# Optimization experiments

Measured on AMD Instinct MI355X. Metric: run time of the kernel, lower is better.

## Reference

```python
import jax, jax.numpy as jnp
import numpy as np

N_REGION = 36
N_PARTIAL = 5
SMOOTH = 9.0
EPS = 1e-8
BN_EPS = 1e-5
LN_EPS = 1e-5


def l2norm(x, axis=-1):
    return x / (jnp.sqrt(jnp.sum(x * x, axis=axis, keepdims=True)) + EPS)


def _uniform_linear(key, fan_in, fan_out):
    r = float(np.sqrt(6.0) / np.sqrt(fan_in + fan_out))
    return jax.random.uniform(key, (fan_in, fan_out), minval=-r, maxval=r, dtype=jnp.float32)


def setup_inputs() -> dict:
    key = jax.random.key(0)
    D, S = 1024, 256
    NI, NC, NW = 64, 32, 40
    ks = jax.random.split(key, 16)
    return {
        "img_emb": jax.random.normal(ks[0], (NI, N_REGION, D), jnp.float32),
        "cap_emb": jax.random.normal(ks[1], (NC, NW, D), jnp.float32),
        "cap_lens": jnp.full((NC,), NW, dtype=jnp.int32),
        "adjs": jax.random.randint(ks[2], (NI, N_REGION, N_REGION), 0, 2).astype(jnp.int32),
        "depends": jnp.zeros((NC, 2), jnp.int32),
        # TextSA (t_global_w)
        "tsa_lw": _uniform_linear(ks[3], D, D), "tsa_lb": jnp.zeros((D,), jnp.float32),
        "tsa_gw": _uniform_linear(ks[4], D, D), "tsa_gb": jnp.zeros((D,), jnp.float32),
        "tsa_cw": _uniform_linear(ks[5], D, 1), "tsa_cb": jnp.zeros((1,), jnp.float32),
        # VisualSA block
        "vl_w": _uniform_linear(ks[6], D, D), "vl_b": jnp.zeros((D,), jnp.float32),
        "vbn_lg": jnp.ones((N_REGION,), jnp.float32), "vbn_lb": jnp.zeros((N_REGION,), jnp.float32),
        "vg_w": _uniform_linear(ks[7], D, D), "vg_b": jnp.zeros((D,), jnp.float32),
        "vbn_gg": jnp.ones((D,), jnp.float32), "vbn_gb": jnp.zeros((D,), jnp.float32),
        "vc_w": _uniform_linear(ks[8], D, 1), "vc_b": jnp.zeros((1,), jnp.float32),
        # similarity heads
        "loc_w": _uniform_linear(ks[9], D, S), "loc_b": jnp.zeros((S,), jnp.float32),
        "par_w": _uniform_linear(ks[10], D, S), "par_b": jnp.zeros((S,), jnp.float32),
        "glo_w": _uniform_linear(ks[11], D, S), "glo_b": jnp.zeros((S,), jnp.float32),
        "sim_w": _uniform_linear(ks[12], S, 1), "sim_b": jnp.zeros((1,), jnp.float32),
        "ln_g": jnp.ones((N_REGION,), jnp.float32), "ln_b": jnp.zeros((N_REGION,), jnp.float32),
    }


def reference(img_emb, cap_emb, cap_lens, adjs, depends,
              tsa_lw, tsa_lb, tsa_gw, tsa_gb, tsa_cw, tsa_cb,
              vl_w, vl_b, vbn_lg, vbn_lb, vg_w, vg_b, vbn_gg, vbn_gb, vc_w, vc_b,
              loc_w, loc_b, par_w, par_b, glo_w, glo_b, sim_w, sim_b, ln_g, ln_b):
    # cap_lens: all captions use the full (uniform) length; depends unused (as in original forward).
    B, R, D = img_emb.shape
    # ---- global image embedding (VisualSA; dropout=identity, BN uses batch stats) ----
    img_ave = img_emb.mean(axis=1)                                    # (B,D)
    h = img_emb @ vl_w + vl_b                                         # (B,R,D)
    mu = h.mean(axis=(0, 2), keepdims=True)
    var = h.var(axis=(0, 2), keepdims=True)
    l_emb = jnp.tanh((h - mu) / jnp.sqrt(var + BN_EPS) * vbn_lg[None, :, None] + vbn_lb[None, :, None])
    g = img_ave @ vg_w + vg_b                                         # (B,D)
    g_emb = jnp.tanh((g - g.mean(0)) / jnp.sqrt(g.var(0) + BN_EPS) * vbn_gg + vbn_gb)
    common = l_emb * g_emb[:, None, :]
    weights_raw = common @ vc_w + vc_b                                # (B,R,1)
    w = jax.nn.softmax(weights_raw[..., 0], axis=-1)[..., None]
    new_global = (w * img_emb).sum(axis=1)                            # (B,D)
    norm_glo = jnp.sqrt(jnp.sum(new_global ** 2, axis=-1, keepdims=True)) + EPS  # (B,1)
    img_glo = new_global / norm_glo                                   # (B,D)
    # ---- partial image embeddings (collect_emb, expressed as direct gather) ----
    vals, idx = jax.lax.top_k(adjs, N_PARTIAL)                        # (B,R,K)
    self_idx = jnp.broadcast_to(jnp.arange(R)[None, :, None], idx.shape)
    eff = jnp.where(vals == 1, idx, self_idx)                         # (B,R,K)
    bidx = jnp.arange(B)[:, None, None]
    feat_g = img_emb[bidx, eff]                                       # (B,R,K,D)
    wg = jax.nn.softmax(weights_raw[bidx, eff][..., 0], axis=-1)[..., None]  # (B,R,K,1)
    img_par = (wg * feat_g).sum(axis=2) / norm_glo[:, None, :]        # (B,R,D)

    def per_cap(cap_i):                                               # cap_i: (NW,D)
        # TextSA global caption embedding (dropout=identity)
        cap_ave = cap_i.mean(axis=0)
        le = jnp.tanh(cap_i @ tsa_lw + tsa_lb)                        # (NW,D)
        ge = jnp.tanh(cap_ave @ tsa_gw + tsa_gb)                      # (D,)
        cw = jax.nn.softmax((le * ge) @ tsa_cw[:, 0] + tsa_cb[0], axis=0)
        cap_glo = l2norm((cw[:, None] * cap_i).sum(axis=0))           # (D,)
        # SCAN attention: query=img_emb, context=caption words (shared across images)
        attn = jnp.einsum('nd,brd->bnr', cap_i, img_emb)              # (B,NW,R)
        attn = jax.nn.leaky_relu(attn, 0.1)
        attn = l2norm(attn, axis=2)
        attn = jax.nn.softmax(attn.transpose(0, 2, 1) * SMOOTH, axis=2)  # (B,R,NW)
        ctx = l2norm(jnp.einsum('brn,nd->brd', attn, cap_i))          # (B,R,D)
        sim_loc = l2norm(jax.nn.relu((ctx - img_emb) ** 2 @ loc_w + loc_b))        # (B,R,S)
        sim_par = l2norm(jax.nn.relu((img_par - cap_glo) ** 2 @ par_w + par_b))    # (B,R,S)
        sim_glo = l2norm(jax.nn.relu((img_glo - cap_glo) ** 2 @ glo_w + glo_b))    # (B,S)
        similarity = sim_par * sim_glo[:, None, :]
        wts = (similarity @ sim_w)[..., 0] + sim_b[0]                 # (B,R)
        m = wts.mean(axis=-1, keepdims=True)
        v = wts.var(axis=-1, keepdims=True)
        wts = jax.nn.sigmoid((wts - m) / jnp.sqrt(v + LN_EPS) * ln_g + ln_b)
        sim_loc = wts[..., None] * sim_loc
        sim_emb = jnp.concatenate([sim_glo[:, None, :], sim_loc], axis=1)  # (B,R+1,S)
        return sim_emb, sim_glo

    sim_emb_v, sim_glo_v = jax.vmap(per_cap)(cap_emb)                 # (NC,B,R+1,S), (NC,B,S)
    return sim_emb_v, sim_glo_v
```

## Files before the change

kernel.cpp:

```cpp
#include <hip/hip_runtime.h>

typedef unsigned short u16;
typedef __attribute__((ext_vector_type(8))) short short8;
typedef __attribute__((ext_vector_type(4))) float f32x4;

#define BN_ 64
#define CN_ 32
#define WN_ 40
#define RN_ 36
#define DN_ 1024
#define SN_ 256
#define KN_ 5
#define EPS_ 1e-8f
#define BNE_ 1e-5f
#define LNE_ 1e-5f
#define SMOOTH_ 9.0f

__device__ __forceinline__ float bf2f(u16 u){ return __uint_as_float(((unsigned)u)<<16); }
__device__ __forceinline__ u16 f2bf(float f){
  unsigned u = __float_as_uint(f);
  u += 0x7fffu + ((u>>16)&1u);
  return (u16)(u>>16);
}
__device__ __forceinline__ float ldf(const void* p, size_t i, int mode){
  return mode ? ((const float*)p)[i] : bf2f(((const u16*)p)[i]);
}
__device__ __forceinline__ void stf(void* p, size_t i, float v, int mode){
  if (mode) ((float*)p)[i] = v; else ((u16*)p)[i] = f2bf(v);
}
__device__ __forceinline__ int get_mode(const unsigned* oneflag){
  return (oneflag[0] == 0x3F800000u) ? 1 : 0;
}
__device__ __forceinline__ short8 ld_frag8(const void* p, size_t elem, int mode){
  if (mode == 0){
    union { uint4 u; short8 s; } cv;
    cv.u = *(const uint4*)((const u16*)p + elem);
    return cv.s;
  } else {
    const float* f = (const float*)p;
    short8 r;
#pragma unroll
    for (int j=0;j<8;j++) r[j] = (short)f2bf(f[elem+j]);
    return r;
  }
}

__device__ __forceinline__ float wave_sum(float v){
#pragma unroll
  for (int off=32; off>0; off>>=1) v += __shfl_down(v, off, 64);
  return v;
}
__device__ float block_sum(float v, float* sc4){
  v = wave_sum(v);
  if ((threadIdx.x & 63)==0) sc4[threadIdx.x>>6] = v;
  __syncthreads();
  float r = sc4[0]+sc4[1]+sc4[2]+sc4[3];
  __syncthreads();
  return r;
}

__global__ void mean_k(const void* X, float* out, int G, int L, float inv, const unsigned* oneflag){
  int mode = get_mode(oneflag);
  int idx = blockIdx.x*256 + threadIdx.x;
  if (idx >= G*DN_) return;
  int g = idx >> 10, d = idx & 1023;
  size_t base = (size_t)g*L*DN_ + d;
  float s = 0.f;
  for (int l=0; l<L; l++) s += ldf(X, base + (size_t)l*DN_, mode);
  out[idx] = s*inv;
}

__global__ void prep_w_k(const void* W, u16* WT, int nlog2, const unsigned* oneflag){
  int mode = get_mode(oneflag);
  int N = 1 << nlog2;
  int idx = blockIdx.x*256 + threadIdx.x;
  if (idx >= (DN_<<nlog2)) return;
  int k = idx >> nlog2, n = idx & (N-1);
  float v = ldf(W, idx, mode);
  WT[(((size_t)(k>>6))*N + n)*64 + (k&63)] = f2bf(v);
}

__global__ __launch_bounds__(256) void gemm_nt_mfma_k(
    const void* A, const void* B, int bt, const u16* WT,
    const void* bias, int has_bias, int act, const unsigned* oneflag,
    float* C, int M, int N, int K){
  int mode = get_mode(oneflag);
  int t = threadIdx.x;
  int w = t>>6, lane = t&63, q = lane>>4, cm = lane&15;
  int m0 = blockIdx.y*64, n0 = blockIdx.x*64 + w*16;
  f32x4 acc[4];
#pragma unroll
  for (int mt=0;mt<4;mt++) acc[mt] = (f32x4){0.f,0.f,0.f,0.f};
  int nkt = K>>6;
  for (int kt=0; kt<nkt; kt++){
#pragma unroll
    for (int ks=0; ks<2; ks++){
      int kb = kt*64 + ks*32 + q*8;
      short8 b;
      if (bt) b = ld_frag8(B, (size_t)(n0+cm)*K + kb, mode);
      else {
        union { uint4 u; short8 s; } cv;
        cv.u = *(const uint4*)(WT + (((size_t)kt*N + n0+cm)*64 + ks*32 + q*8));
        b = cv.s;
      }
#pragma unroll
      for (int mt=0; mt<4; mt++){
        short8 a = ld_frag8(A, (size_t)(m0+mt*16+cm)*K + kb, mode);
        acc[mt] = __builtin_amdgcn_mfma_f32_16x16x32_bf16(a, b, acc[mt], 0,0,0);
      }
    }
  }
  float bv = has_bias ? ldf(bias, n0+cm, mode) : 0.f;
#pragma unroll
  for (int mt=0; mt<4; mt++){
#pragma unroll
    for (int r=0; r<4; r++){
      int m = m0 + mt*16 + q*4 + r;
      float v = acc[mt][r] + bv;
      if (act==1) v = tanhf(v);
      C[(size_t)m*N + n0+cm] = v;
    }
  }
}

__global__ void bnl_sum_k(const float* h, float* bnp){
  __shared__ float sc[4];
  int r = blockIdx.x>>3, bg = blockIdx.x&7;
  float s=0.f, s2=0.f;
  for (int bb=0; bb<8; bb++){
    int b = bg*8+bb;
    const float* p = h + ((size_t)b*RN_ + r)*DN_;
    for (int d=threadIdx.x; d<DN_; d+=256){ float x=p[d]; s+=x; s2+=x*x; }
  }
  s  = block_sum(s,  sc);
  s2 = block_sum(s2, sc);
  if (threadIdx.x==0){ bnp[blockIdx.x*2]=s; bnp[blockIdx.x*2+1]=s2; }
}
__global__ void bnl_apply_k(float* h, const void* gg_, const void* bb_,
                            const float* bnp, const unsigned* oneflag){
  int mode = get_mode(oneflag);
  int row = blockIdx.x; int r = row % RN_;
  float s=0.f, s2=0.f;
  for (int j=0;j<8;j++){ s += bnp[(r*8+j)*2]; s2 += bnp[(r*8+j)*2+1]; }
  float inv = 1.f/(float)(BN_*DN_);
  float mu = s*inv;
  float var = s2*inv - mu*mu;
  float rstd = rsqrtf(var + BNE_);
  float gg = ldf(gg_, r, mode), bb = ldf(bb_, r, mode);
  float* p = h + (size_t)row*DN_;
  for (int d=threadIdx.x; d<DN_; d+=256) p[d] = tanhf((p[d]-mu)*rstd*gg + bb);
}

__global__ void bn_global_k(float* g, const void* gg_, const void* bb_, const unsigned* oneflag){
  int mode = get_mode(oneflag);
  int d = blockIdx.x*256 + threadIdx.x;
  if (d >= DN_) return;
  float s=0.f, s2=0.f;
  for (int b=0;b<BN_;b++){ float x=g[(size_t)b*DN_+d]; s+=x; s2+=x*x; }
  float m = s/(float)BN_;
  float var = s2/(float)BN_ - m*m;
  float rstd = rsqrtf(var + BNE_);
  float ga=ldf(gg_,d,mode), be=ldf(bb_,d,mode);
  for (int b=0;b<BN_;b++){
    size_t i=(size_t)b*DN_+d;
    g[i] = tanhf((g[i]-m)*rstd*ga + be);
  }
}

__global__ void gemm_k(const void* A, int a_ws, const void* B, int transb,
                       const void* bias, int has_bias, int act,
                       const unsigned* oneflag, float* C, int M, int N, int K){
  __shared__ float As[32][33];
  __shared__ float Bs[32][33];
  int mode = get_mode(oneflag);
  int n0 = blockIdx.x*32, m0 = blockIdx.y*32;
  int tid = threadIdx.x;
  int tx = tid & 15, ty = tid >> 4;
  float a00=0,a01=0,a10=0,a11=0;
  for (int kt=0; kt<K; kt+=32){
    for (int l=0; l<4; l++){
      int idx = tid + l*256;
      {
        int i = idx >> 5, k = idx & 31;
        int m = m0 + i;
        float v = 0.f;
        if (m < M){
          size_t off = (size_t)m*K + kt + k;
          v = a_ws ? ((const float*)A)[off] : ldf(A, off, mode);
        }
        As[i][k] = v;
      }
      if (!transb){
        int k = idx >> 5, j = idx & 31;
        int n = n0 + j;
        Bs[k][j] = (n<N) ? ldf(B, (size_t)(kt+k)*N + n, mode) : 0.f;
      } else {
        int j = idx >> 5, k = idx & 31;
        int n = n0 + j;
        Bs[k][j] = (n<N) ? ldf(B, (size_t)n*K + kt + k, mode) : 0.f;
      }
    }
    __syncthreads();
#pragma unroll
    for (int kk=0; kk<32; kk++){
      float x0 = As[ty][kk], x1 = As[ty+16][kk];
      float y0 = Bs[kk][tx], y1 = Bs[kk][tx+16];
      a00 += x0*y0; a01 += x0*y1; a10 += x1*y0; a11 += x1*y1;
    }
    __syncthreads();
  }
  float acc[2][2] = {{a00,a01},{a10,a11}};
  for (int i=0;i<2;i++){
    for (int j=0;j<2;j++){
      int m = m0 + ty + i*16, n = n0 + tx + j*16;
      if (m<M && n<N){
        float v = acc[i][j];
        if (has_bias) v += ldf(bias, n, mode);
        if (act==1) v = tanhf(v);
        C[(size_t)m*N + n] = v;
      }
    }
  }
}

__global__ void wraw_k(const float* lemb, const float* gemb, const void* vc_w, const void* vc_b,
                       float* wraw, const unsigned* oneflag){
  __shared__ float sc[4];
  int mode = get_mode(oneflag);
  int br = blockIdx.x; int b = br / RN_;
  const float* lp = lemb + (size_t)br*DN_;
  const float* gp = gemb + (size_t)b*DN_;
  float s=0.f;
  for (int d=threadIdx.x; d<DN_; d+=256) s += lp[d]*gp[d]*ldf(vc_w,d,mode);
  s = block_sum(s, sc);
  if (threadIdx.x==0) wraw[br] = s + ldf(vc_b,0,mode);
}

__global__ void glo_k(const float* wraw, const void* img, float* img_glo, float* rnorm,
                      const unsigned* oneflag){
  __shared__ float sc[4];
  __shared__ float wsm[RN_];
  __shared__ float srn;
  int mode = get_mode(oneflag);
  int b = blockIdx.x;
  if (threadIdx.x==0){
    float mx=-1e30f;
    for (int r=0;r<RN_;r++) mx = fmaxf(mx, wraw[b*RN_+r]);
    float sum=0.f;
    for (int r=0;r<RN_;r++){ float e=expf(wraw[b*RN_+r]-mx); wsm[r]=e; sum+=e; }
    float inv=1.f/sum;
    for (int r=0;r<RN_;r++) wsm[r]*=inv;
  }
  __syncthreads();
  float ng[4]; float s2=0.f;
#pragma unroll
  for (int j=0;j<4;j++){
    int d = threadIdx.x + j*256;
    float s=0.f;
    for (int r=0;r<RN_;r++) s += wsm[r]*ldf(img, ((size_t)b*RN_+r)*DN_ + d, mode);
    ng[j]=s; s2 += s*s;
  }
  s2 = block_sum(s2, sc);
  if (threadIdx.x==0) srn = 1.f/(sqrtf(s2)+EPS_);
  __syncthreads();
  float rn = srn;
#pragma unroll
  for (int j=0;j<4;j++) img_glo[(size_t)b*DN_ + threadIdx.x + j*256] = ng[j]*rn;
  if (threadIdx.x==0) rnorm[b]=rn;
}

__global__ void partial_k(const float* wraw, const int* adjs, const void* img,
                          const float* rnorm, u16* img_parh, const unsigned* oneflag){
  __shared__ float wg[KN_];
  __shared__ int eff[KN_];
  int mode = get_mode(oneflag);
  int br = blockIdx.x; int b = br / RN_; int r = br % RN_;
  if (threadIdx.x==0){
    int cnt=0;
    const int* ap = adjs + (size_t)br*RN_;
    for (int j=0;j<RN_ && cnt<KN_;j++) if (ap[j]==1) eff[cnt++]=j;
    for (int k=cnt;k<KN_;k++) eff[k]=r;
    float v[KN_]; float mx=-1e30f;
    for (int k=0;k<KN_;k++){ v[k]=wraw[b*RN_+eff[k]]; mx=fmaxf(mx,v[k]); }
    float sum=0.f;
    for (int k=0;k<KN_;k++){ v[k]=expf(v[k]-mx); sum+=v[k]; }
    float inv=1.f/sum;
    for (int k=0;k<KN_;k++) wg[k]=v[k]*inv;
  }
  __syncthreads();
  float rn = rnorm[b];
  for (int d=threadIdx.x; d<DN_; d+=256){
    float s=0.f;
#pragma unroll
    for (int k=0;k<KN_;k++) s += wg[k]*ldf(img, ((size_t)b*RN_+eff[k])*DN_ + d, mode);
    img_parh[(size_t)br*DN_ + d] = f2bf(s*rn);
  }
}

__global__ void capglo_k(const float* le, const float* ge, const void* tsa_cw, const void* tsa_cb,
                         const void* cap, float* cap_glo, const unsigned* oneflag){
  __shared__ float sc[4];
  __shared__ float score[WN_];
  __shared__ float srn;
  int mode = get_mode(oneflag);
  int c = blockIdx.x;
  int t = threadIdx.x;
  float gw[4];
#pragma unroll
  for (int j=0;j<4;j++){ int d=t+j*256; gw[j] = ge[(size_t)c*DN_+d]*ldf(tsa_cw,d,mode); }
  float cb0 = ldf(tsa_cb,0,mode);
  for (int n=0;n<WN_;n++){
    const float* lp = le + ((size_t)c*WN_+n)*DN_;
    float s=0.f;
#pragma unroll
    for (int j=0;j<4;j++) s += lp[t+j*256]*gw[j];
    s = block_sum(s, sc);
    if (t==0) score[n] = s + cb0;
  }
  __syncthreads();
  if (t==0){
    float mx=-1e30f;
    for (int n=0;n<WN_;n++) mx=fmaxf(mx,score[n]);
    float sum=0.f;
    for (int n=0;n<WN_;n++){ float e=expf(score[n]-mx); score[n]=e; sum+=e; }
    float inv=1.f/sum;
    for (int n=0;n<WN_;n++) score[n]*=inv;
  }
  __syncthreads();
  float v[4]; float s2=0.f;
#pragma unroll
  for (int j=0;j<4;j++){
    int d=t+j*256;
    float s=0.f;
    for (int n=0;n<WN_;n++) s += score[n]*ldf(cap, ((size_t)c*WN_+n)*DN_ + d, mode);
    v[j]=s; s2+=s*s;
  }
  s2 = block_sum(s2, sc);
  if (t==0) srn = 1.f/(sqrtf(s2)+EPS_);
  __syncthreads();
#pragma unroll
  for (int j=0;j<4;j++) cap_glo[(size_t)c*DN_ + t + j*256] = v[j]*srn;
}

__global__ void attn_norm_k(float* attn){
  __shared__ float buf[BN_*RN_];
  int row = blockIdx.x;
  int t = threadIdx.x;
  float* p = attn + (size_t)row*(BN_*RN_);
  for (int i=t; i<BN_*RN_; i+=256){
    float x = p[i];
    buf[i] = (x>=0.f)? x : 0.1f*x;
  }
  __syncthreads();
  if (t < BN_){
    float s2=0.f;
#pragma unroll
    for (int r=0;r<RN_;r++){ float x=buf[t*RN_+r]; s2+=x*x; }
    float rn = 1.f/(sqrtf(s2)+EPS_);
#pragma unroll
    for (int r=0;r<RN_;r++) buf[t*RN_+r] *= rn;
  }
  __syncthreads();
  for (int i=t; i<BN_*RN_; i+=256) p[i] = buf[i];
}

__global__ void gram_k(const void* cap, float* gram, const unsigned* oneflag){
  __shared__ float capS[WN_][128];
  int mode = get_mode(oneflag);
  int c = blockIdx.x, t = threadIdx.x;
  float acc[7];
  int pi[7], pj[7];
#pragma unroll
  for (int u=0; u<7; u++){
    acc[u]=0.f;
    int p = t + u*256;
    pi[u] = p/40; pj[u] = p%40;
    if (pi[u] >= WN_) pi[u] = 0;
  }
  for (int k0=0; k0<DN_; k0+=128){
    for (int i=t; i<WN_*128; i+=256){
      int n = i>>7, kk = i&127;
      capS[n][kk] = ldf(cap, ((size_t)c*WN_+n)*DN_ + k0+kk, mode);
    }
    __syncthreads();
#pragma unroll
    for (int u=0; u<7; u++){
      if (t + u*256 < 1600){
        float s=0.f;
        for (int kk=0; kk<128; kk++) s += capS[pi[u]][kk]*capS[pj[u]][kk];
        acc[u] += s;
      }
    }
    __syncthreads();
  }
#pragma unroll
  for (int u=0; u<7; u++)
    if (t + u*256 < 1600) gram[(size_t)c*1600 + t + u*256] = acc[u];
}

__global__ void simglo_k(const float* img_glo, const float* cap_glo, const void* glo_w,
                         const void* glo_b, float* simglo_ws, void* out, const unsigned* oneflag){
  __shared__ float X[DN_];
  __shared__ float sc[4];
  __shared__ float srn;
  int mode = get_mode(oneflag);
  int cb = blockIdx.x; int c = cb >> 6; int b = cb & 63;
  int t = threadIdx.x;
#pragma unroll
  for (int j=0;j<4;j++){
    int d=t+j*256;
    float dif = img_glo[(size_t)b*DN_+d] - cap_glo[(size_t)c*DN_+d];
    X[d] = dif*dif;
  }
  __syncthreads();
  float acc=0.f;
  for (int k=0;k<DN_;k++) acc += X[k]*ldf(glo_w, (size_t)k*SN_ + t, mode);
  acc += ldf(glo_b, t, mode);
  acc = fmaxf(acc, 0.f);
  float s2 = block_sum(acc*acc, sc);
  if (t==0) srn = 1.f/(sqrtf(s2)+EPS_);
  __syncthreads();
  float o = acc*srn;
  simglo_ws[(size_t)cb*SN_ + t] = o;
  stf(out, (size_t)cb*37*SN_ + t, o, mode);
  stf(out, (size_t)CN_*BN_*37*SN_ + (size_t)cb*SN_ + t, o, mode);
}

__global__ __launch_bounds__(256) void wts_mfma_k(const u16* img_parh, const float* cap_glo,
    const u16* WT, const void* par_b, const float* simglo, const void* sim_w,
    const void* sim_b, float* wts_raw, const unsigned* oneflag){
  __shared__ uint4 AsV[2][512];
  __shared__ float red[4][64];
  __shared__ float rns[64];
  int mode = get_mode(oneflag);
  int t = threadIdx.x;
  int rows0 = blockIdx.x*64;
  int c = rows0 / (BN_*RN_);
  int br0 = rows0 % (BN_*RN_);
  int w = t>>6, lane = t&63, q = lane>>4, cm = lane&15;
  f32x4 acc[4][4];
#pragma unroll
  for (int mt=0;mt<4;mt++)
#pragma unroll
    for (int nt=0;nt<4;nt++) acc[mt][nt] = (f32x4){0.f,0.f,0.f,0.f};

  for (int kt=0; kt<16; kt++){
    int p = kt&1;
#pragma unroll
    for (int h=0; h<2; h++){
      int fi = t + h*256;
      int mt = fi>>7, ks=(fi>>6)&1, ln=fi&63;
      int fq = ln>>4, fcm = ln&15;
      int row = mt*16+fcm;
      int kb = kt*64 + ks*32 + fq*8;
      union { uint4 u; u16 s[8]; } pv;
      pv.u = *(const uint4*)(img_parh + (size_t)(br0+row)*DN_ + kb);
      const float* cg = cap_glo + (size_t)c*DN_ + kb;
      union { uint4 u; u16 s[8]; } xs;
#pragma unroll
      for (int j=0;j<8;j++){ float d = bf2f(pv.s[j]) - cg[j]; xs.s[j] = f2bf(d*d); }
      AsV[p][fi & 511] = xs.u;
    }
    __syncthreads();
#pragma unroll
    for (int ks=0; ks<2; ks++){
      short8 a[4];
#pragma unroll
      for (int mt=0; mt<4; mt++){
        union { uint4 u; short8 s; } cv;
        cv.u = AsV[p][(mt*2+ks)*64 + lane];
        a[mt] = cv.s;
      }
#pragma unroll
      for (int nt=0; nt<4; nt++){
        int n = w*64 + nt*16 + cm;
        union { uint4 u; short8 s; } bv;
        bv.u = *(const uint4*)(WT + (((size_t)kt*SN_ + n)*64 + ks*32 + q*8));
#pragma unroll
        for (int mt=0; mt<4; mt++)
          acc[mt][nt] = __builtin_amdgcn_mfma_f32_16x16x32_bf16(a[mt], bv.s, acc[mt][nt], 0,0,0);
      }
    }
  }
  int sarr[4]; float sw[4];
#pragma unroll
  for (int nt=0; nt<4; nt++){
    int s = w*64+nt*16+cm;
    sarr[nt] = s;
    float pb = ldf(par_b, s, mode);
    sw[nt] = ldf(sim_w, s, mode);
#pragma unroll
    for (int mt=0;mt<4;mt++)
#pragma unroll
      for (int r=0;r<4;r++) acc[mt][nt][r] = fmaxf(acc[mt][nt][r]+pb, 0.f);
  }
#pragma unroll
  for (int mt=0;mt<4;mt++)
#pragma unroll
  for (int r=0;r<4;r++){
    float v=0.f;
#pragma unroll
    for (int nt=0;nt<4;nt++) v += acc[mt][nt][r]*acc[mt][nt][r];
    v += __shfl_xor(v,1,64); v += __shfl_xor(v,2,64);
    v += __shfl_xor(v,4,64); v += __shfl_xor(v,8,64);
    if (cm==0) red[w][mt*16+q*4+r] = v;
  }
  __syncthreads();
  if (t<64) rns[t] = 1.f/(sqrtf(red[0][t]+red[1][t]+red[2][t]+red[3][t])+EPS_);
  __syncthreads();
#pragma unroll
  for (int mt=0;mt<4;mt++)
#pragma unroll
  for (int r=0;r<4;r++){
    int rowl = mt*16+q*4+r;
    int br = br0+rowl; int b = br/RN_; int cb = c*BN_+b;
    float v=0.f;
#pragma unroll
    for (int nt=0;nt<4;nt++) v += acc[mt][nt][r]*simglo[(size_t)cb*SN_+sarr[nt]]*sw[nt];
    v += __shfl_xor(v,1,64); v += __shfl_xor(v,2,64);
    v += __shfl_xor(v,4,64); v += __shfl_xor(v,8,64);
    if (cm==0) red[w][rowl] = v;
  }
  __syncthreads();
  if (t<64) wts_raw[rows0+t] = (red[0][t]+red[1][t]+red[2][t]+red[3][t])*rns[t] + ldf(sim_b,0,mode);
}

__global__ void ln_k(const float* wts_raw, const void* ln_g, const void* ln_b,
                     float* wts_f, const unsigned* oneflag){
  int mode = get_mode(oneflag);
  int cb = blockIdx.x*256 + threadIdx.x;
  if (cb >= CN_*BN_) return;
  const float* p = wts_raw + (size_t)cb*RN_;
  float s=0.f, s2=0.f;
#pragma unroll
  for (int r=0;r<RN_;r++){ float x=p[r]; s+=x; s2+=x*x; }
  float m = s/(float)RN_;
  float v = s2/(float)RN_ - m*m;
  float rstd = rsqrtf(v + LNE_);
  float* q = wts_f + (size_t)cb*RN_;
#pragma unroll
  for (int r=0;r<RN_;r++){
    float x = (p[r]-m)*rstd*ldf(ln_g,r,mode) + ldf(ln_b,r,mode);
    q[r] = 1.f/(1.f+expf(-x));
  }
}

__global__ __launch_bounds__(256) void simloc_mfma_k(const float* attnr, const void* cap,
    const void* img, const u16* WT, const void* loc_b, const float* wts_f,
    const float* gram, void* out, const unsigned* oneflag){
  __shared__ float A40s[64][41];
  __shared__ u16 Ps[64][72];
  __shared__ u16 capT[64][72];
  __shared__ u16 Xs[64][72];
  __shared__ float Gc[WN_*WN_];
  __shared__ float crn[64];
  __shared__ float red[4][64];
  __shared__ float rns[64];
  int mode = get_mode(oneflag);
  int t = threadIdx.x;
  int rows0 = blockIdx.x*64;
  int c = rows0 / (BN_*RN_);
  int br0 = rows0 % (BN_*RN_);
  int w = t>>6, lane = t&63, q = lane>>4, cm = lane&15;

  for (int i=t; i<64*WN_; i+=256){
    int rr = i&63, n = i>>6;
    A40s[rr][n] = attnr[((size_t)c*WN_+n)*(BN_*RN_) + br0 + rr];
  }
  for (int i=t; i<WN_*WN_; i+=256) Gc[i] = gram[(size_t)c*1600 + i];
  for (int i=t; i<64*24; i+=256){
    int ke = i/24, wd = 40 + (i - ke*24);
    capT[ke][wd] = 0;
  }
  __syncthreads();
  if (t < 64){
    float mx=-1e30f;
#pragma unroll
    for (int n=0;n<WN_;n++) mx = fmaxf(mx, A40s[t][n]);
    float sum=0.f;
    float e[WN_];
#pragma unroll
    for (int n=0;n<WN_;n++){ e[n]=expf(SMOOTH_*(A40s[t][n]-mx)); sum+=e[n]; }
    float inv=1.f/sum;
#pragma unroll
    for (int n=0;n<WN_;n++){ float pv=e[n]*inv; A40s[t][n]=pv; Ps[t][n]=f2bf(pv); }
#pragma unroll
    for (int n=WN_;n<64;n++) Ps[t][n]=0;
  }
  __syncthreads();
  {
    int row = t>>2, pp = t&3;
    float gs = 0.f;
    for (int i=0;i<WN_;i++){
      float ai = A40s[row][i];
      float ps = 0.f;
      for (int j=pp; j<WN_; j+=4) ps += A40s[row][j]*Gc[i*WN_+j];
      gs += ai*ps;
    }
    gs += __shfl_xor(gs,1,64); gs += __shfl_xor(gs,2,64);
    if (pp==0) crn[row] = 1.f/(sqrtf(fmaxf(gs,0.f))+EPS_);
  }

  f32x4 acc[4][4];
#pragma unroll
  for (int mt=0;mt<4;mt++)
#pragma unroll
    for (int nt=0;nt<4;nt++) acc[mt][nt] = (f32x4){0.f,0.f,0.f,0.f};
  __syncthreads();

  for (int kt=0; kt<16; kt++){
    for (int i=t; i<WN_*8; i+=256){
      int wd = i>>3, kg = i&7;
      short8 cv = ld_frag8(cap, ((size_t)c*WN_+wd)*DN_ + kt*64 + kg*8, mode);
#pragma unroll
      for (int j=0;j<8;j++) capT[kg*8+j][wd] = (u16)cv[j];
    }
    __syncthreads();
    f32x4 ctxacc[4];
#pragma unroll
    for (int mt=0;mt<4;mt++) ctxacc[mt] = (f32x4){0.f,0.f,0.f,0.f};
#pragma unroll
    for (int ks=0; ks<2; ks++){
      union { uint4 u; short8 s; } bv;
      bv.u = *(const uint4*)(&capT[w*16+cm][ks*32+q*8]);
#pragma unroll
      for (int mt=0; mt<4; mt++){
        union { uint4 u; short8 s; } av;
        av.u = *(const uint4*)(&Ps[mt*16+cm][ks*32+q*8]);
        ctxacc[mt] = __builtin_amdgcn_mfma_f32_16x16x32_bf16(av.s, bv.s, ctxacc[mt], 0,0,0);
      }
    }
#pragma unroll
    for (int mt=0; mt<4; mt++){
#pragma unroll
      for (int r=0; r<4; r++){
        int row = mt*16 + q*4 + r;
        float iv = ldf(img, (size_t)(br0+row)*DN_ + kt*64 + w*16 + cm, mode);
        float x = ctxacc[mt][r]*crn[row] - iv;
        Xs[row][w*16+cm] = f2bf(x*x);
      }
    }
    __syncthreads();
#pragma unroll
    for (int ks=0; ks<2; ks++){
      short8 a[4];
#pragma unroll
      for (int mt=0; mt<4; mt++){
        union { uint4 u; short8 s; } av;
        av.u = *(const uint4*)(&Xs[mt*16+cm][ks*32+q*8]);
        a[mt] = av.s;
      }
#pragma unroll
      for (int nt=0; nt<4; nt++){
        int n = w*64 + nt*16 + cm;
        union { uint4 u; short8 s; } bv;
        bv.u = *(const uint4*)(WT + (((size_t)kt*SN_ + n)*64 + ks*32 + q*8));
#pragma unroll
        for (int mt=0; mt<4; mt++)
          acc[mt][nt] = __builtin_amdgcn_mfma_f32_16x16x32_bf16(a[mt], bv.s, acc[mt][nt], 0,0,0);
      }
    }
    __syncthreads();
  }
  int sarr[4];
#pragma unroll
  for (int nt=0; nt<4; nt++){
    int s = w*64+nt*16+cm;
    sarr[nt] = s;
    float lb = ldf(loc_b, s, mode);
#pragma unroll
    for (int mt=0;mt<4;mt++)
#pragma unroll
      for (int r=0;r<4;r++) acc[mt][nt][r] = fmaxf(acc[mt][nt][r]+lb, 0.f);
  }
#pragma unroll
  for (int mt=0;mt<4;mt++)
#pragma unroll
  for (int r=0;r<4;r++){
    float v=0.f;
#pragma unroll
    for (int nt=0;nt<4;nt++) v += acc[mt][nt][r]*acc[mt][nt][r];
    v += __shfl_xor(v,1,64); v += __shfl_xor(v,2,64);
    v += __shfl_xor(v,4,64); v += __shfl_xor(v,8,64);
    if (cm==0) red[w][mt*16+q*4+r] = v;
  }
  __syncthreads();
  if (t<64) rns[t] = 1.f/(sqrtf(red[0][t]+red[1][t]+red[2][t]+red[3][t])+EPS_);
  __syncthreads();
#pragma unroll
  for (int mt=0;mt<4;mt++)
#pragma unroll
  for (int r=0;r<4;r++){
    int rowl = mt*16+q*4+r;
    int br = br0+rowl; int b = br/RN_; int rr = br%RN_; int cb = c*BN_+b;
    float scl = rns[rowl]*wts_f[rows0+rowl];
    size_t obase = ((size_t)(cb*37) + 1 + rr)*SN_;
#pragma unroll
    for (int nt=0;nt<4;nt++) stf(out, obase + sarr[nt], acc[mt][nt][r]*scl, mode);
  }
}

extern "C" void kernel_launch(void* const* d_in, const int* in_sizes, int n_in,
                              void* d_out, int out_size, void* d_ws, size_t ws_size,
                              hipStream_t stream) {
  const void* img    = d_in[0];
  const void* cap    = d_in[1];
  const int*  adjs   = (const int*)d_in[3];
  const void* tsa_lw = d_in[5];
  const void* tsa_lb = d_in[6];
  const void* tsa_gw = d_in[7];
  const void* tsa_gb = d_in[8];
  const void* tsa_cw = d_in[9];
  const void* tsa_cb = d_in[10];
  const void* vl_w   = d_in[11];
  const void* vl_b   = d_in[12];
  const void* vbn_lg = d_in[13];
  const void* vbn_lb = d_in[14];
  const void* vg_w   = d_in[15];
  const void* vg_b   = d_in[16];
  const void* vbn_gg = d_in[17];
  const void* vbn_gb = d_in[18];
  const void* vc_w   = d_in[19];
  const void* vc_b   = d_in[20];
  const void* loc_w  = d_in[21];
  const void* loc_b  = d_in[22];
  const void* par_w  = d_in[23];
  const void* par_b  = d_in[24];
  const void* glo_w  = d_in[25];
  const void* glo_b  = d_in[26];
  const void* sim_w  = d_in[27];
  const void* sim_b  = d_in[28];
  const void* ln_g   = d_in[29];
  const void* ln_b   = d_in[30];
  const unsigned* oneflag = (const unsigned*)d_in[29];
  void* out = d_out;

  float* f = (float*)d_ws;
  float* U        = f;
  float* H        = U;
  float* LE       = U + 2359296;
  float* ATTNR    = U;
  float* IMG_PARHf= U        + 3670016;
  float* IMG_AVE  = IMG_PARHf+ 1179648;
  float* G        = IMG_AVE  + 65536;
  float* WRAW     = G        + 65536;
  float* RNORM    = WRAW     + 2304;
  float* IMG_GLO  = RNORM    + 64;
  float* CAP_AVE  = IMG_GLO  + 65536;
  float* GE       = CAP_AVE  + 32768;
  float* CAP_GLO  = GE       + 32768;
  float* SIMGLO   = CAP_GLO  + 32768;
  float* WTSR     = SIMGLO   + 524288;
  float* WTSF     = WTSR     + 73728;
  float* WTLOCf   = WTSF     + 73728;
  float* WTPARf   = WTLOCf   + 131072;
  float* WTVLf    = WTPARf   + 131072;
  float* WTTLf    = WTVLf    + 524288;
  float* GRAM     = WTTLf    + 524288;
  float* BNP      = GRAM     + 51200;
  u16* IMG_PARH = (u16*)IMG_PARHf;
  u16* WT_LOC = (u16*)WTLOCf;
  u16* WT_PAR = (u16*)WTPARf;
  u16* WT_VL  = (u16*)WTVLf;
  u16* WT_TL  = (u16*)WTTLf;

  prep_w_k<<<1024, 256, 0, stream>>>(loc_w, WT_LOC, 8, oneflag);
  prep_w_k<<<1024, 256, 0, stream>>>(par_w, WT_PAR, 8, oneflag);
  prep_w_k<<<4096, 256, 0, stream>>>(vl_w,  WT_VL, 10, oneflag);
  prep_w_k<<<4096, 256, 0, stream>>>(tsa_lw,WT_TL, 10, oneflag);
  gram_k<<<CN_, 256, 0, stream>>>(cap, GRAM, oneflag);

  mean_k<<<256, 256, 0, stream>>>(img, IMG_AVE, BN_, RN_, 1.f/RN_, oneflag);
  mean_k<<<128, 256, 0, stream>>>(cap, CAP_AVE, CN_, WN_, 1.f/WN_, oneflag);
  gemm_nt_mfma_k<<<dim3(16,36), 256, 0, stream>>>(img, (const void*)0, 0, WT_VL,
      vl_b, 1, 0, oneflag, H, BN_*RN_, DN_, DN_);
  bnl_sum_k<<<RN_*8, 256, 0, stream>>>(H, BNP);
  bnl_apply_k<<<BN_*RN_, 256, 0, stream>>>(H, vbn_lg, vbn_lb, BNP, oneflag);
  gemm_k<<<dim3(32,2), 256, 0, stream>>>(IMG_AVE, 1, vg_w, 0, vg_b, 1, 0, oneflag, G, BN_, DN_, DN_);
  bn_global_k<<<4, 256, 0, stream>>>(G, vbn_gg, vbn_gb, oneflag);
  wraw_k<<<BN_*RN_, 256, 0, stream>>>(H, G, vc_w, vc_b, WRAW, oneflag);
  glo_k<<<BN_, 256, 0, stream>>>(WRAW, img, IMG_GLO, RNORM, oneflag);
  partial_k<<<BN_*RN_, 256, 0, stream>>>(WRAW, adjs, img, RNORM, IMG_PARH, oneflag);

  gemm_nt_mfma_k<<<dim3(16,20), 256, 0, stream>>>(cap, (const void*)0, 0, WT_TL,
      tsa_lb, 1, 1, oneflag, LE, CN_*WN_, DN_, DN_);
  gemm_k<<<dim3(32,1), 256, 0, stream>>>(CAP_AVE, 1, tsa_gw, 0, tsa_gb, 1, 1, oneflag, GE, CN_, DN_, DN_);
  capglo_k<<<CN_, 256, 0, stream>>>(LE, GE, tsa_cw, tsa_cb, cap, CAP_GLO, oneflag);
  gemm_nt_mfma_k<<<dim3(36,20), 256, 0, stream>>>(cap, img, 1, (const u16*)0,
      (const void*)0, 0, 0, oneflag, ATTNR, CN_*WN_, BN_*RN_, DN_);
  attn_norm_k<<<CN_*WN_, 256, 0, stream>>>(ATTNR);

  simglo_k<<<CN_*BN_, 256, 0, stream>>>(IMG_GLO, CAP_GLO, glo_w, glo_b, SIMGLO, out, oneflag);
  wts_mfma_k<<<CN_*BN_*RN_/64, 256, 0, stream>>>(IMG_PARH, CAP_GLO, WT_PAR, par_b, SIMGLO, sim_w, sim_b, WTSR, oneflag);
  ln_k<<<8, 256, 0, stream>>>(WTSR, ln_g, ln_b, WTSF, oneflag);
  simloc_mfma_k<<<CN_*BN_*RN_/64, 256, 0, stream>>>(ATTNR, cap, img, WT_LOC, loc_b, WTSF, GRAM, out, oneflag);
}
```

Before: 1.931 ms.

## Pre-transpose caption tiles and double-buffer simloc ctx computation with register-held P

A new kernel writes the caption embeddings once as bf16 in a per-tile transposed layout. simloc_mfma_k then loads these tiles with vector copies into double-buffered shared memory, prefetching the next tile, instead of doing scalar transposes every k-step. The softmax matrix is kept in registers as the B fragment, image values are loaded four at a time, and one barrier per iteration is dropped. wts_mfma_k also reads a bf16 copy of cap_glo, which rounds cap_glo before the subtraction and adds a small precision difference.

```diff
diff --git a/kernel.cpp b/kernel.cpp
--- a/kernel.cpp
+++ b/kernel.cpp
@@ -44,6 +44,17 @@
     return r;
   }
 }
+__device__ __forceinline__ void ld4f(const void* p, size_t off, int mode, float* o){
+  if (mode==0){
+    uint2 v = *(const uint2*)((const u16*)p + off);
+    o[0]=bf2f((u16)(v.x&0xffffu)); o[1]=bf2f((u16)(v.x>>16));
+    o[2]=bf2f((u16)(v.y&0xffffu)); o[3]=bf2f((u16)(v.y>>16));
+  } else {
+    const float* f=(const float*)p + off;
+#pragma unroll
+    for (int j=0;j<4;j++) o[j]=f[j];
+  }
+}
 
 __device__ __forceinline__ float wave_sum(float v){
 #pragma unroll
@@ -78,6 +89,30 @@
   int k = idx >> nlog2, n = idx & (N-1);
   float v = ldf(W, idx, mode);
   WT[(((size_t)(k>>6))*N + n)*64 + (k&63)] = f2bf(v);
+}
+
+__global__ void prep_capt_k(const void* cap, u16* capTG, const unsigned* oneflag){
+  __shared__ u16 tile[WN_][72];
+  int mode = get_mode(oneflag);
+  int blk = blockIdx.x; int c = blk>>4, kt = blk&15;
+  int t = threadIdx.x;
+  if (mode==0){
+    for (int i=t; i<WN_*8; i+=256){
+      int wd=i>>3, ch=i&7;
+      uint4 v = *(const uint4*)((const u16*)cap + ((size_t)(c*WN_+wd)*DN_ + kt*64 + ch*8));
+      *(uint4*)&tile[wd][ch*8] = v;
+    }
+  } else {
+    for (int i=t; i<WN_*64; i+=256){
+      int wd=i>>6, e=i&63;
+      tile[wd][e] = f2bf(((const float*)cap)[(size_t)(c*WN_+wd)*DN_ + kt*64 + e]);
+    }
+  }
+  __syncthreads();
+  for (int i=t; i<64*WN_; i+=256){
+    int kelem=i/WN_, wd=i-kelem*WN_;
+    capTG[((size_t)(c*16+kt)*64 + kelem)*WN_ + wd] = tile[wd][kelem];
+  }
 }
 
 __global__ __launch_bounds__(256) void gemm_nt_mfma_k(
@@ -298,7 +333,7 @@
 }
 
 __global__ void capglo_k(const float* le, const float* ge, const void* tsa_cw, const void* tsa_cb,
-                         const void* cap, float* cap_glo, const unsigned* oneflag){
+                         const void* cap, float* cap_glo, u16* cap_glo_h, const unsigned* oneflag){
   __shared__ float sc[4];
   __shared__ float score[WN_];
   __shared__ float srn;
@@ -339,7 +374,11 @@
   if (t==0) srn = 1.f/(sqrtf(s2)+EPS_);
   __syncthreads();
 #pragma unroll
-  for (int j=0;j<4;j++) cap_glo[(size_t)c*DN_ + t + j*256] = v[j]*srn;
+  for (int j=0;j<4;j++){
+    float o = v[j]*srn;
+    cap_glo[(size_t)c*DN_ + t + j*256] = o;
+    cap_glo_h[(size_t)c*DN_ + t + j*256] = f2bf(o);
+  }
 }
 
 __global__ void attn_norm_k(float* attn){
@@ -426,7 +465,7 @@
   stf(out, (size_t)CN_*BN_*37*SN_ + (size_t)cb*SN_ + t, o, mode);
 }
 
-__global__ __launch_bounds__(256) void wts_mfma_k(const u16* img_parh, const float* cap_glo,
+__global__ __launch_bounds__(256) void wts_mfma_k(const u16* img_parh, const u16* cap_glo_h,
     const u16* WT, const void* par_b, const float* simglo, const void* sim_w,
     const void* sim_b, float* wts_raw, const unsigned* oneflag){
   __shared__ uint4 AsV[2][512];
@@ -453,12 +492,11 @@
       int fq = ln>>4, fcm = ln&15;
       int row = mt*16+fcm;
       int kb = kt*64 + ks*32 + fq*8;
-      union { uint4 u; u16 s[8]; } pv;
+      union { uint4 u; u16 s[8]; } pv, cv, xs;
       pv.u = *(const uint4*)(img_parh + (size_t)(br0+row)*DN_ + kb);
-      const float* cg = cap_glo + (size_t)c*DN_ + kb;
-      union { uint4 u; u16 s[8]; } xs;
-#pragma unroll
-      for (int j=0;j<8;j++){ float d = bf2f(pv.s[j]) - cg[j]; xs.s[j] = f2bf(d*d); }
+      cv.u = *(const uint4*)(cap_glo_h + (size_t)c*DN_ + kb);
+#pragma unroll
+      for (int j=0;j<8;j++){ float d = bf2f(pv.s[j]) - bf2f(cv.s[j]); xs.s[j] = f2bf(d*d); }
       AsV[p][fi & 511] = xs.u;
     }
     __syncthreads();
@@ -545,17 +583,29 @@
   }
 }
 
-__global__ __launch_bounds__(256) void simloc_mfma_k(const float* attnr, const void* cap,
+#define SM_CAPT   0
+#define SM_XS     18432
+#define SM_A40    0
+#define SM_GC     10496
+#define SM_PST    36864
+#define SM_CRN    46080
+#define SM_RED    46336
+#define SM_RNS    47360
+#define SM_TOTAL  47616
+
+__global__ __launch_bounds__(256) void simloc_mfma_k(const float* attnr, const u16* capTG,
     const void* img, const u16* WT, const void* loc_b, const float* wts_f,
     const float* gram, void* out, const unsigned* oneflag){
-  __shared__ float A40s[64][41];
-  __shared__ u16 Ps[64][72];
-  __shared__ u16 capT[64][72];
-  __shared__ u16 Xs[64][72];
-  __shared__ float Gc[WN_*WN_];
-  __shared__ float crn[64];
-  __shared__ float red[4][64];
-  __shared__ float rns[64];
+  __shared__ char smem[SM_TOTAL];
+  u16*   capT = (u16*)(smem + SM_CAPT);
+  u16*   Xs   = (u16*)(smem + SM_XS);
+  float* A40  = (float*)(smem + SM_A40);
+  float* Gc   = (float*)(smem + SM_GC);
+  u16*   PsT  = (u16*)(smem + SM_PST);
+  float* crn  = (float*)(smem + SM_CRN);
+  float* red  = (float*)(smem + SM_RED);
+  float* rns  = (float*)(smem + SM_RNS);
+
   int mode = get_mode(oneflag);
   int t = threadIdx.x;
   int rows0 = blockIdx.x*64;
@@ -565,41 +615,59 @@
 
   for (int i=t; i<64*WN_; i+=256){
     int rr = i&63, n = i>>6;
-    A40s[rr][n] = attnr[((size_t)c*WN_+n)*(BN_*RN_) + br0 + rr];
+    A40[rr*41+n] = attnr[((size_t)c*WN_+n)*(BN_*RN_) + br0 + rr];
   }
   for (int i=t; i<WN_*WN_; i+=256) Gc[i] = gram[(size_t)c*1600 + i];
-  for (int i=t; i<64*24; i+=256){
-    int ke = i/24, wd = 40 + (i - ke*24);
-    capT[ke][wd] = 0;
-  }
   __syncthreads();
   if (t < 64){
     float mx=-1e30f;
 #pragma unroll
-    for (int n=0;n<WN_;n++) mx = fmaxf(mx, A40s[t][n]);
+    for (int n=0;n<WN_;n++) mx = fmaxf(mx, A40[t*41+n]);
     float sum=0.f;
     float e[WN_];
 #pragma unroll
-    for (int n=0;n<WN_;n++){ e[n]=expf(SMOOTH_*(A40s[t][n]-mx)); sum+=e[n]; }
+    for (int n=0;n<WN_;n++){ e[n]=expf(SMOOTH_*(A40[t*41+n]-mx)); sum+=e[n]; }
     float inv=1.f/sum;
 #pragma unroll
-    for (int n=0;n<WN_;n++){ float pv=e[n]*inv; A40s[t][n]=pv; Ps[t][n]=f2bf(pv); }
-#pragma unroll
-    for (int n=WN_;n<64;n++) Ps[t][n]=0;
+    for (int n=0;n<WN_;n++){ float pv=e[n]*inv; A40[t*41+n]=pv; PsT[n*72+t]=f2bf(pv); }
+#pragma unroll
+    for (int n=WN_;n<64;n++) PsT[n*72+t]=0;
   }
   __syncthreads();
   {
     int row = t>>2, pp = t&3;
     float gs = 0.f;
     for (int i=0;i<WN_;i++){
-      float ai = A40s[row][i];
+      float ai = A40[row*41+i];
       float ps = 0.f;
-      for (int j=pp; j<WN_; j+=4) ps += A40s[row][j]*Gc[i*WN_+j];
+      for (int j=pp; j<WN_; j+=4) ps += A40[row*41+j]*Gc[i*WN_+j];
       gs += ai*ps;
     }
     gs += __shfl_xor(gs,1,64); gs += __shfl_xor(gs,2,64);
     if (pp==0) crn[row] = 1.f/(sqrtf(fmaxf(gs,0.f))+EPS_);
   }
+  __syncthreads();
+
+  short8 bP[2];
+#pragma unroll
+  for (int ks2=0; ks2<2; ks2++)
+#pragma unroll
+    for (int j=0;j<8;j++) bP[ks2][j] = (short)PsT[(ks2*32+q*8+j)*72 + w*16+cm];
+
+  for (int i=t; i<2*64*24; i+=256){
+    int buf = i/1536, rem = i - buf*1536;
+    int kelem = rem/24, wd = 40 + rem - (rem/24)*24;
+    capT[((size_t)(buf*64+kelem))*72 + wd] = 0;
+  }
+  for (int i=t; i<320; i+=256){
+    int kelem = i/5, wc = i - kelem*5;
+    uint4 v = *(const uint4*)(capTG + (((size_t)(c*16+0)*64 + kelem)*WN_ + wc*8));
+    *(uint4*)(capT + (size_t)kelem*72 + wc*8) = v;
+  }
+  float cr = 0.f;
+  {
+    cr = crn[w*16+cm];
+  }
 
   f32x4 acc[4][4];
 #pragma unroll
@@ -609,45 +677,51 @@
   __syncthreads();
 
   for (int kt=0; kt<16; kt++){
-    for (int i=t; i<WN_*8; i+=256){
-      int wd = i>>3, kg = i&7;
-      short8 cv = ld_frag8(cap, ((size_t)c*WN_+wd)*DN_ + kt*64 + kg*8, mode);
-#pragma unroll
-      for (int j=0;j<8;j++) capT[kg*8+j][wd] = (u16)cv[j];
+    int p = kt&1;
+    if (kt < 15){
+      int pn = p^1;
+      for (int i=t; i<320; i+=256){
+        int kelem = i/5, wc = i - kelem*5;
+        uint4 v = *(const uint4*)(capTG + (((size_t)(c*16+kt+1)*64 + kelem)*WN_ + wc*8));
+        *(uint4*)(capT + ((size_t)(pn*64+kelem))*72 + wc*8) = v;
+      }
+    }
+    f32x4 ctxacc[4];
+#pragma unroll
+    for (int mt2=0;mt2<4;mt2++) ctxacc[mt2] = (f32x4){0.f,0.f,0.f,0.f};
+#pragma unroll
+    for (int ks2=0; ks2<2; ks2++){
+#pragma unroll
+      for (int mt2=0; mt2<4; mt2++){
+        union { uint4 u; short8 s; } av;
+        av.u = *(const uint4*)(capT + ((size_t)(p*64+mt2*16+cm))*72 + ks2*32 + q*8);
+        ctxacc[mt2] = __builtin_amdgcn_mfma_f32_16x16x32_bf16(av.s, bP[ks2], ctxacc[mt2], 0,0,0);
+      }
+    }
+    int rowg = w*16+cm;
+#pragma unroll
+    for (int mt2=0; mt2<4; mt2++){
+      float iv[4];
+      ld4f(img, (size_t)(br0+rowg)*DN_ + kt*64 + mt2*16 + q*4, mode, iv);
+      u16 xa[4];
+#pragma unroll
+      for (int r=0;r<4;r++){
+        float x = ctxacc[mt2][r]*cr - iv[r];
+        xa[r] = f2bf(x*x);
+      }
+      uint2 pk;
+      pk.x = (unsigned)xa[0] | ((unsigned)xa[1]<<16);
+      pk.y = (unsigned)xa[2] | ((unsigned)xa[3]<<16);
+      *(uint2*)(Xs + ((size_t)(p*64+rowg))*72 + mt2*16 + q*4) = pk;
     }
     __syncthreads();
-    f32x4 ctxacc[4];
-#pragma unroll
-    for (int mt=0;mt<4;mt++) ctxacc[mt] = (f32x4){0.f,0.f,0.f,0.f};
 #pragma unroll
     for (int ks=0; ks<2; ks++){
-      union { uint4 u; short8 s; } bv;
-      bv.u = *(const uint4*)(&capT[w*16+cm][ks*32+q*8]);
+      short8 a[4];
 #pragma unroll
       for (int mt=0; mt<4; mt++){
         union { uint4 u; short8 s; } av;
-        av.u = *(const uint4*)(&Ps[mt*16+cm][ks*32+q*8]);
-        ctxacc[mt] = __builtin_amdgcn_mfma_f32_16x16x32_bf16(av.s, bv.s, ctxacc[mt], 0,0,0);
-      }
-    }
-#pragma unroll
-    for (int mt=0; mt<4; mt++){
-#pragma unroll
-      for (int r=0; r<4; r++){
-        int row = mt*16 + q*4 + r;
-        float iv = ldf(img, (size_t)(br0+row)*DN_ + kt*64 + w*16 + cm, mode);
-        float x = ctxacc[mt][r]*crn[row] - iv;
-        Xs[row][w*16+cm] = f2bf(x*x);
-      }
-    }
-    __syncthreads();
-#pragma unroll
-    for (int ks=0; ks<2; ks++){
-      short8 a[4];
-#pragma unroll
-      for (int mt=0; mt<4; mt++){
-        union { uint4 u; short8 s; } av;
-        av.u = *(const uint4*)(&Xs[mt*16+cm][ks*32+q*8]);
+        av.u = *(const uint4*)(Xs + ((size_t)(p*64+mt*16+cm))*72 + ks*32 + q*8);
         a[mt] = av.s;
       }
 #pragma unroll
@@ -660,7 +734,6 @@
           acc[mt][nt] = __builtin_amdgcn_mfma_f32_16x16x32_bf16(a[mt], bv.s, acc[mt][nt], 0,0,0);
       }
     }
-    __syncthreads();
   }
   int sarr[4];
 #pragma unroll
@@ -682,10 +755,10 @@
     for (int nt=0;nt<4;nt++) v += acc[mt][nt][r]*acc[mt][nt][r];
     v += __shfl_xor(v,1,64); v += __shfl_xor(v,2,64);
     v += __shfl_xor(v,4,64); v += __shfl_xor(v,8,64);
-    if (cm==0) red[w][mt*16+q*4+r] = v;
-  }
-  __syncthreads();
-  if (t<64) rns[t] = 1.f/(sqrtf(red[0][t]+red[1][t]+red[2][t]+red[3][t])+EPS_);
+    if (cm==0) red[w*64 + mt*16+q*4+r] = v;
+  }
+  __syncthreads();
+  if (t<64) rns[t] = 1.f/(sqrtf(red[t]+red[64+t]+red[128+t]+red[192+t])+EPS_);
   __syncthreads();
 #pragma unroll
   for (int mt=0;mt<4;mt++)
@@ -740,6 +813,7 @@
   float* H        = U;
   float* LE       = U + 2359296;
   float* ATTNR    = U;
+  float* CAPTGf   = U + 2949120;
   float* IMG_PARHf= U        + 3670016;
   float* IMG_AVE  = IMG_PARHf+ 1179648;
   float* G        = IMG_AVE  + 65536;
@@ -758,11 +832,14 @@
   float* WTTLf    = WTVLf    + 524288;
   float* GRAM     = WTTLf    + 524288;
   float* BNP      = GRAM     + 51200;
+  float* CAPGLOHf = BNP      + 576;
   u16* IMG_PARH = (u16*)IMG_PARHf;
   u16* WT_LOC = (u16*)WTLOCf;
   u16* WT_PAR = (u16*)WTPARf;
   u16* WT_VL  = (u16*)WTVLf;
   u16* WT_TL  = (u16*)WTTLf;
+  u16* CAPTG  = (u16*)CAPTGf;
+  u16* CAPGLOH= (u16*)CAPGLOHf;
 
   prep_w_k<<<1024, 256, 0, stream>>>(loc_w, WT_LOC, 8, oneflag);
   prep_w_k<<<1024, 256, 0, stream>>>(par_w, WT_PAR, 8, oneflag);
@@ -785,13 +862,14 @@
   gemm_nt_mfma_k<<<dim3(16,20), 256, 0, stream>>>(cap, (const void*)0, 0, WT_TL,
       tsa_lb, 1, 1, oneflag, LE, CN_*WN_, DN_, DN_);
   gemm_k<<<dim3(32,1), 256, 0, stream>>>(CAP_AVE, 1, tsa_gw, 0, tsa_gb, 1, 1, oneflag, GE, CN_, DN_, DN_);
-  capglo_k<<<CN_, 256, 0, stream>>>(LE, GE, tsa_cw, tsa_cb, cap, CAP_GLO, oneflag);
+  capglo_k<<<CN_, 256, 0, stream>>>(LE, GE, tsa_cw, tsa_cb, cap, CAP_GLO, CAPGLOH, oneflag);
+  prep_capt_k<<<CN_*16, 256, 0, stream>>>(cap, CAPTG, oneflag);
   gemm_nt_mfma_k<<<dim3(36,20), 256, 0, stream>>>(cap, img, 1, (const u16*)0,
       (const void*)0, 0, 0, oneflag, ATTNR, CN_*WN_, BN_*RN_, DN_);
   attn_norm_k<<<CN_*WN_, 256, 0, stream>>>(ATTNR);
 
   simglo_k<<<CN_*BN_, 256, 0, stream>>>(IMG_GLO, CAP_GLO, glo_w, glo_b, SIMGLO, out, oneflag);
-  wts_mfma_k<<<CN_*BN_*RN_/64, 256, 0, stream>>>(IMG_PARH, CAP_GLO, WT_PAR, par_b, SIMGLO, sim_w, sim_b, WTSR, oneflag);
+  wts_mfma_k<<<CN_*BN_*RN_/64, 256, 0, stream>>>(IMG_PARH, CAPGLOH, WT_PAR, par_b, SIMGLO, sim_w, sim_b, WTSR, oneflag);
   ln_k<<<8, 256, 0, stream>>>(WTSR, ln_g, ln_b, WTSF, oneflag);
-  simloc_mfma_k<<<CN_*BN_*RN_/64, 256, 0, stream>>>(ATTNR, cap, img, WT_LOC, loc_b, WTSF, GRAM, out, oneflag);
-}
+  simloc_mfma_k<<<CN_*BN_*RN_/64, 256, 0, stream>>>(ATTNR, CAPTG, img, WT_LOC, loc_b, WTSF, GRAM, out, oneflag);
+}
```

New measurement: 1.734 ms. 10.2% less time.
